# Kernel tuning notes

Hardware: AMD Instinct MI355X
Metric: run time of the kernel (lower is better)

The kernel has to match this reference:

```python
import jax, jax.numpy as jnp
import numpy as np

S = 7          # grid cells per side (CFG['CELL_NUMS'])
L_COORD = 5.0  # CFG['L_COORD']
L_NOOBJ = 0.5  # CFG['L_NOOBJ']
N_BATCH = 16384


def setup_inputs() -> dict:
    key = jax.random.key(0)
    k1, k2, k3 = jax.random.split(key, 3)
    pred = jax.random.uniform(k1, (N_BATCH, S, S, 30), dtype=jnp.float32)
    target = jax.random.uniform(k2, (N_BATCH, S, S, 30), dtype=jnp.float32)
    obj = jax.random.uniform(k3, (N_BATCH, S, S)) < 0.3
    target = target.at[..., 4].set(jnp.where(obj, target[..., 4], 0.0))
    target = target.at[..., 9].set(jnp.where(obj, target[..., 9], 0.0))
    return {"pred_tensor": pred, "target_tensor": target}


def _yolo_v1_loss(pred, target):
    # pred/target: [N, S, S, 30] = [2 boxes x (x,y,w,h,c), 20 class probs]
    N = pred.shape[0]
    coo_f = (target[..., 4] > 0).astype(pred.dtype)   # [N,S,S] object cells
    noo_f = 1.0 - coo_f                                # no-object cells

    # no-object loss: confidence channels 4 and 9 on noo cells (sum-MSE)
    nooobj_loss = jnp.sum(
        noo_f * ((pred[..., 4] - target[..., 4]) ** 2
                 + (pred[..., 9] - target[..., 9]) ** 2))

    # class loss over object cells (sum-MSE over 20 classes)
    class_loss = jnp.sum(coo_f[..., None] * (pred[..., 10:] - target[..., 10:]) ** 2)

    # boxes: [N,S,S,2,5]
    pb = pred[..., :10].reshape(N, S, S, 2, 5)
    tb = target[..., :10].reshape(N, S, S, 2, 5)

    # xywh -> xyxy for the 2 predicted boxes and the first target box per cell
    p_lt = pb[..., :2] - 0.5 * pb[..., 2:4]
    p_rb = pb[..., :2] + 0.5 * pb[..., 2:4]
    t0 = tb[..., 0, :]                                 # target box used for IOU
    t_lt = t0[..., :2] - 0.5 * t0[..., 2:4]
    t_rb = t0[..., :2] + 0.5 * t0[..., 2:4]

    # NOTE: faithful reproduction of the source's compute_iou, including its
    # bug: wh = (rb - lt < 0).float(), so 'inter' is an indicator product.
    lt = jnp.maximum(p_lt, t_lt[..., None, :])         # [N,S,S,2,2]
    rb = jnp.minimum(p_rb, t_rb[..., None, :])
    wh_ind = (rb - lt < 0).astype(pred.dtype)
    inter = wh_ind[..., 0] * wh_ind[..., 1]            # [N,S,S,2]
    area1 = (p_rb[..., 0] - p_lt[..., 0]) * (p_rb[..., 1] - p_lt[..., 1])
    area2 = ((t_rb[..., 0] - t_lt[..., 0]) * (t_rb[..., 1] - t_lt[..., 1]))[..., None]
    iou = inter / (area1 + area2 - inter)              # [N,S,S,2]

    # responsible box = argmax IOU over the 2 predicted boxes per cell
    idx = jnp.argmax(iou, axis=-1)                     # [N,S,S]
    gather = idx[..., None, None]                      # [N,S,S,1,1]
    resp_p = jnp.take_along_axis(pb, gather, axis=3)[..., 0, :]  # [N,S,S,5]
    resp_t = jnp.take_along_axis(tb, gather, axis=3)[..., 0, :]

    contain_loss = jnp.sum(coo_f * (resp_p[..., 4] - resp_t[..., 4]) ** 2)

    # guard sqrt at masked-out cells so 0*d(sqrt(0)) does not produce NaN grads
    safe = coo_f[..., None] > 0
    sqrt_wp = jnp.sqrt(jnp.where(safe, resp_p[..., 2:4], 1.0))
    sqrt_wt = jnp.sqrt(jnp.where(safe, resp_t[..., 2:4], 1.0))
    loc_loss = (jnp.sum(coo_f[..., None] * (resp_p[..., :2] - resp_t[..., :2]) ** 2)
                + jnp.sum(coo_f[..., None] * (sqrt_wp - sqrt_wt) ** 2))

    return (L_COORD * loc_loss + contain_loss + L_NOOBJ * nooobj_loss + class_loss) / N


def reference(pred_tensor, target_tensor):
    return _yolo_v1_loss(pred_tensor, target_tensor)
```

## Files before the change

### kernel.cpp

```cpp
#include <hip/hip_runtime.h>


#define CH 30
#define CPB 256
#define T 256
#define TILE_F (CPB * CH)
#define TILE_V4 (TILE_F / 4)

typedef __attribute__((address_space(3))) void* lds_vp;
typedef const __attribute__((address_space(1))) void* gvp;

__global__ __launch_bounds__(T, 4)
void yolo_partial(const float* __restrict__ pred,
                  const float* __restrict__ targ,
                  float* __restrict__ partial) {
    __shared__ float tile[TILE_F];
    __shared__ float wave_sums[T / 64];

    const int tid = threadIdx.x;
    const long long fbase = (long long)blockIdx.x * TILE_F;

    {
        const float4* gt = (const float4*)(targ + fbase);
#pragma unroll
        for (int k = 0; k < 8; ++k) {
            const int v = tid + k * T;
            if (v < TILE_V4)
                __builtin_amdgcn_global_load_lds((gvp)(gt + v), (lds_vp)(tile + v * 4),
                                                 16, 0, 0);
        }
    }
    __syncthreads();

    float2 t01, t23, t45, t67, t89, tc[10];
    {
        const float2* t2 = (const float2*)(tile + tid * CH);
        t01 = t2[0]; t23 = t2[1]; t45 = t2[2]; t67 = t2[3]; t89 = t2[4];
#pragma unroll
        for (int k = 0; k < 10; ++k) tc[k] = t2[5 + k];
    }
    __syncthreads();

    {
        const float4* gp = (const float4*)(pred + fbase);
#pragma unroll
        for (int k = 0; k < 8; ++k) {
            const int v = tid + k * T;
            if (v < TILE_V4)
                __builtin_amdgcn_global_load_lds((gvp)(gp + v), (lds_vp)(tile + v * 4),
                                                 16, 0, 0);
        }
    }
    __syncthreads();

    float sum = 0.0f;
    {
        const float2* p2 = (const float2*)(tile + tid * CH);
        const float2 p01 = p2[0], p23 = p2[1], p45 = p2[2], p67 = p2[3], p89 = p2[4];

        const float t4 = t45.x, t9 = t89.y;
        const bool coo = t4 > 0.0f;

        const float d4 = p45.x - t4;
        const float d9 = p89.y - t9;
        sum = coo ? 0.0f : 0.5f * (d4 * d4 + d9 * d9);

        if (coo) {
            float cl = 0.0f;
#pragma unroll
            for (int k = 0; k < 10; ++k) {
                const float2 pc = p2[5 + k];
                const float dx = pc.x - tc[k].x;
                const float dy = pc.y - tc[k].y;
                cl += dx * dx + dy * dy;
            }
            sum += cl;

            const float tltx = t01.x - 0.5f * t23.x;
            const float tlty = t01.y - 0.5f * t23.y;
            const float trbx = t01.x + 0.5f * t23.x;
            const float trby = t01.y + 0.5f * t23.y;
            const float area2 = (trbx - tltx) * (trby - tlty);

            const float b0x = p01.x, b0y = p01.y, b0w = p23.x, b0h = p23.y;
            const float b1x = p45.y, b1y = p67.x, b1w = p67.y, b1h = p89.x;

            float iou0, iou1;
            {
                const float pltx = b0x - 0.5f * b0w, plty = b0y - 0.5f * b0h;
                const float prbx = b0x + 0.5f * b0w, prby = b0y + 0.5f * b0h;
                const float ltx = fmaxf(pltx, tltx), lty = fmaxf(plty, tlty);
                const float rbx = fminf(prbx, trbx), rby = fminf(prby, trby);
                const float inter = ((rbx - ltx < 0.0f) ? 1.0f : 0.0f) *
                                    ((rby - lty < 0.0f) ? 1.0f : 0.0f);
                const float area1 = (prbx - pltx) * (prby - plty);
                iou0 = inter / (area1 + area2 - inter);
            }
            {
                const float pltx = b1x - 0.5f * b1w, plty = b1y - 0.5f * b1h;
                const float prbx = b1x + 0.5f * b1w, prby = b1y + 0.5f * b1h;
                const float ltx = fmaxf(pltx, tltx), lty = fmaxf(plty, tlty);
                const float rbx = fminf(prbx, trbx), rby = fminf(prby, trby);
                const float inter = ((rbx - ltx < 0.0f) ? 1.0f : 0.0f) *
                                    ((rby - lty < 0.0f) ? 1.0f : 0.0f);
                const float area1 = (prbx - pltx) * (prby - plty);
                iou1 = inter / (area1 + area2 - inter);
            }
            const bool idx1 = iou1 > iou0;

            const float rpx = idx1 ? b1x : b0x;
            const float rpy = idx1 ? b1y : b0y;
            const float rpw = idx1 ? b1w : b0w;
            const float rph = idx1 ? b1h : b0h;
            const float rpc = idx1 ? p89.y : p45.x;
            const float rtx = idx1 ? t45.y : t01.x;
            const float rty = idx1 ? t67.x : t01.y;
            const float rtw = idx1 ? t67.y : t23.x;
            const float rth = idx1 ? t89.x : t23.y;
            const float rtc = idx1 ? t89.y : t45.x;

            const float dc = rpc - rtc;
            sum += dc * dc;

            const float dx = rpx - rtx;
            const float dy = rpy - rty;
            const float dw = sqrtf(rpw) - sqrtf(rtw);
            const float dh = sqrtf(rph) - sqrtf(rth);
            sum += 5.0f * (dx * dx + dy * dy + dw * dw + dh * dh);
        }
    }

#pragma unroll
    for (int off = 32; off > 0; off >>= 1)
        sum += __shfl_down(sum, off, 64);
    const int wave = tid >> 6;
    const int lane = tid & 63;
    if (lane == 0) wave_sums[wave] = sum;
    __syncthreads();
    if (tid == 0) {
        float tot = 0.0f;
#pragma unroll
        for (int w = 0; w < T / 64; ++w) tot += wave_sums[w];
        partial[blockIdx.x] = tot;
    }
}

__global__ __launch_bounds__(256)
void yolo_reduce(const float* __restrict__ partial, int n, float* __restrict__ out) {
    __shared__ float wave_sums[4];
    float s = 0.0f;
    const int n4 = n >> 2;
    const float4* p4 = (const float4*)partial;
    for (int v = threadIdx.x; v < n4; v += 256) {
        const float4 x = p4[v];
        s += (x.x + x.y) + (x.z + x.w);
    }
    for (int v = (n4 << 2) + threadIdx.x; v < n; v += 256)
        s += partial[v];
#pragma unroll
    for (int off = 32; off > 0; off >>= 1)
        s += __shfl_down(s, off, 64);
    const int wave = threadIdx.x >> 6;
    const int lane = threadIdx.x & 63;
    if (lane == 0) wave_sums[wave] = s;
    __syncthreads();
    if (threadIdx.x == 0) {
        const float tot = wave_sums[0] + wave_sums[1] + wave_sums[2] + wave_sums[3];
        out[0] = tot * (1.0f / 16384.0f);
    }
}

extern "C" void kernel_launch(void* const* d_in, const int* in_sizes, int n_in,
                              void* d_out, int out_size, void* d_ws, size_t ws_size,
                              hipStream_t stream) {
    const float* pred = (const float*)d_in[0];
    const float* targ = (const float*)d_in[1];
    float* out = (float*)d_out;
    float* partial = (float*)d_ws;

    const int n_cells = in_sizes[0] / CH;
    const int blocks = n_cells / CPB;

    yolo_partial<<<blocks, T, 0, stream>>>(pred, targ, partial);
    yolo_reduce<<<1, 256, 0, stream>>>(partial, blocks, out);
}
```

Measured before the change: 204.5 us.

## Replace LDS-staged tile loads with direct per-thread global float2 loads

Drops the global_load_lds staging of target and pred tiles into shared memory, along with the block barriers between stages. Each thread now reads its own cell's 30 floats of target and pred directly from global memory into registers as float2 loads. This removes the LDS round trip and barriers and lets both inputs load concurrently. The cost is strided, uncoalesced per-thread access with a 120-byte stride, which spreads each wave's loads across many cache lines and relies on L2/TA efficiency.

```diff
diff --git a/kernel.cpp b/kernel.cpp
--- a/kernel.cpp
+++ b/kernel.cpp
@@ -2,132 +2,94 @@
 
 
 #define CH 30
-#define CPB 256
 #define T 256
-#define TILE_F (CPB * CH)
-#define TILE_V4 (TILE_F / 4)
-
-typedef __attribute__((address_space(3))) void* lds_vp;
-typedef const __attribute__((address_space(1))) void* gvp;
 
 __global__ __launch_bounds__(T, 4)
 void yolo_partial(const float* __restrict__ pred,
                   const float* __restrict__ targ,
                   float* __restrict__ partial) {
-    __shared__ float tile[TILE_F];
     __shared__ float wave_sums[T / 64];
 
     const int tid = threadIdx.x;
-    const long long fbase = (long long)blockIdx.x * TILE_F;
+    const size_t cell = (size_t)blockIdx.x * T + tid;
 
-    {
-        const float4* gt = (const float4*)(targ + fbase);
+    const float2* t2 = (const float2*)targ + cell * (CH / 2);
+    const float2* p2 = (const float2*)pred + cell * (CH / 2);
+
+    float2 t[15], p[15];
 #pragma unroll
-        for (int k = 0; k < 8; ++k) {
-            const int v = tid + k * T;
-            if (v < TILE_V4)
-                __builtin_amdgcn_global_load_lds((gvp)(gt + v), (lds_vp)(tile + v * 4),
-                                                 16, 0, 0);
+    for (int k = 0; k < 15; ++k) t[k] = t2[k];
+#pragma unroll
+    for (int k = 0; k < 15; ++k) p[k] = p2[k];
+
+    const float t4 = t[2].x, t9 = t[4].y;
+    const bool coo = t4 > 0.0f;
+
+    const float d4 = p[2].x - t4;
+    const float d9 = p[4].y - t9;
+    float sum = coo ? 0.0f : 0.5f * (d4 * d4 + d9 * d9);
+
+    if (coo) {
+        float cl = 0.0f;
+#pragma unroll
+        for (int k = 0; k < 10; ++k) {
+            const float dx = p[5 + k].x - t[5 + k].x;
+            const float dy = p[5 + k].y - t[5 + k].y;
+            cl += dx * dx + dy * dy;
         }
-    }
-    __syncthreads();
+        sum += cl;
 
-    float2 t01, t23, t45, t67, t89, tc[10];
-    {
-        const float2* t2 = (const float2*)(tile + tid * CH);
-        t01 = t2[0]; t23 = t2[1]; t45 = t2[2]; t67 = t2[3]; t89 = t2[4];
-#pragma unroll
-        for (int k = 0; k < 10; ++k) tc[k] = t2[5 + k];
-    }
-    __syncthreads();
+        const float tltx = t[0].x - 0.5f * t[1].x;
+        const float tlty = t[0].y - 0.5f * t[1].y;
+        const float trbx = t[0].x + 0.5f * t[1].x;
+        const float trby = t[0].y + 0.5f * t[1].y;
+        const float area2 = (trbx - tltx) * (trby - tlty);
 
-    {
-        const float4* gp = (const float4*)(pred + fbase);
-#pragma unroll
-        for (int k = 0; k < 8; ++k) {
-            const int v = tid + k * T;
-            if (v < TILE_V4)
-                __builtin_amdgcn_global_load_lds((gvp)(gp + v), (lds_vp)(tile + v * 4),
-                                                 16, 0, 0);
+        const float b0x = p[0].x, b0y = p[0].y, b0w = p[1].x, b0h = p[1].y;
+        const float b1x = p[2].y, b1y = p[3].x, b1w = p[3].y, b1h = p[4].x;
+
+        float iou0, iou1;
+        {
+            const float pltx = b0x - 0.5f * b0w, plty = b0y - 0.5f * b0h;
+            const float prbx = b0x + 0.5f * b0w, prby = b0y + 0.5f * b0h;
+            const float ltx = fmaxf(pltx, tltx), lty = fmaxf(plty, tlty);
+            const float rbx = fminf(prbx, trbx), rby = fminf(prby, trby);
+            const float inter = ((rbx - ltx < 0.0f) ? 1.0f : 0.0f) *
+                                ((rby - lty < 0.0f) ? 1.0f : 0.0f);
+            const float area1 = (prbx - pltx) * (prby - plty);
+            iou0 = inter / (area1 + area2 - inter);
         }
-    }
-    __syncthreads();
+        {
+            const float pltx = b1x - 0.5f * b1w, plty = b1y - 0.5f * b1h;
+            const float prbx = b1x + 0.5f * b1w, prby = b1y + 0.5f * b1h;
+            const float ltx = fmaxf(pltx, tltx), lty = fmaxf(plty, tlty);
+            const float rbx = fminf(prbx, trbx), rby = fminf(prby, trby);
+            const float inter = ((rbx - ltx < 0.0f) ? 1.0f : 0.0f) *
+                                ((rby - lty < 0.0f) ? 1.0f : 0.0f);
+            const float area1 = (prbx - pltx) * (prby - plty);
+            iou1 = inter / (area1 + area2 - inter);
+        }
+        const bool idx1 = iou1 > iou0;
 
-    float sum = 0.0f;
-    {
-        const float2* p2 = (const float2*)(tile + tid * CH);
-        const float2 p01 = p2[0], p23 = p2[1], p45 = p2[2], p67 = p2[3], p89 = p2[4];
+        const float rpx = idx1 ? b1x : b0x;
+        const float rpy = idx1 ? b1y : b0y;
+        const float rpw = idx1 ? b1w : b0w;
+        const float rph = idx1 ? b1h : b0h;
+        const float rpc = idx1 ? p[4].y : p[2].x;
+        const float rtx = idx1 ? t[2].y : t[0].x;
+        const float rty = idx1 ? t[3].x : t[0].y;
+        const float rtw = idx1 ? t[3].y : t[1].x;
+        const float rth = idx1 ? t[4].x : t[1].y;
+        const float rtc = idx1 ? t[4].y : t[2].x;
 
-        const float t4 = t45.x, t9 = t89.y;
-        const bool coo = t4 > 0.0f;
+        const float dc = rpc - rtc;
+        sum += dc * dc;
 
-        const float d4 = p45.x - t4;
-        const float d9 = p89.y - t9;
-        sum = coo ? 0.0f : 0.5f * (d4 * d4 + d9 * d9);
-
-        if (coo) {
-            float cl = 0.0f;
-#pragma unroll
-            for (int k = 0; k < 10; ++k) {
-                const float2 pc = p2[5 + k];
-                const float dx = pc.x - tc[k].x;
-                const float dy = pc.y - tc[k].y;
-                cl += dx * dx + dy * dy;
-            }
-            sum += cl;
-
-            const float tltx = t01.x - 0.5f * t23.x;
-            const float tlty = t01.y - 0.5f * t23.y;
-            const float trbx = t01.x + 0.5f * t23.x;
-            const float trby = t01.y + 0.5f * t23.y;
-            const float area2 = (trbx - tltx) * (trby - tlty);
-
-            const float b0x = p01.x, b0y = p01.y, b0w = p23.x, b0h = p23.y;
-            const float b1x = p45.y, b1y = p67.x, b1w = p67.y, b1h = p89.x;
-
-            float iou0, iou1;
-            {
-                const float pltx = b0x - 0.5f * b0w, plty = b0y - 0.5f * b0h;
-                const float prbx = b0x + 0.5f * b0w, prby = b0y + 0.5f * b0h;
-                const float ltx = fmaxf(pltx, tltx), lty = fmaxf(plty, tlty);
-                const float rbx = fminf(prbx, trbx), rby = fminf(prby, trby);
-                const float inter = ((rbx - ltx < 0.0f) ? 1.0f : 0.0f) *
-                                    ((rby - lty < 0.0f) ? 1.0f : 0.0f);
-                const float area1 = (prbx - pltx) * (prby - plty);
-                iou0 = inter / (area1 + area2 - inter);
-            }
-            {
-                const float pltx = b1x - 0.5f * b1w, plty = b1y - 0.5f * b1h;
-                const float prbx = b1x + 0.5f * b1w, prby = b1y + 0.5f * b1h;
-                const float ltx = fmaxf(pltx, tltx), lty = fmaxf(plty, tlty);
-                const float rbx = fminf(prbx, trbx), rby = fminf(prby, trby);
-                const float inter = ((rbx - ltx < 0.0f) ? 1.0f : 0.0f) *
-                                    ((rby - lty < 0.0f) ? 1.0f : 0.0f);
-                const float area1 = (prbx - pltx) * (prby - plty);
-                iou1 = inter / (area1 + area2 - inter);
-            }
-            const bool idx1 = iou1 > iou0;
-
-            const float rpx = idx1 ? b1x : b0x;
-            const float rpy = idx1 ? b1y : b0y;
-            const float rpw = idx1 ? b1w : b0w;
-            const float rph = idx1 ? b1h : b0h;
-            const float rpc = idx1 ? p89.y : p45.x;
-            const float rtx = idx1 ? t45.y : t01.x;
-            const float rty = idx1 ? t67.x : t01.y;
-            const float rtw = idx1 ? t67.y : t23.x;
-            const float rth = idx1 ? t89.x : t23.y;
-            const float rtc = idx1 ? t89.y : t45.x;
-
-            const float dc = rpc - rtc;
-            sum += dc * dc;
-
-            const float dx = rpx - rtx;
-            const float dy = rpy - rty;
-            const float dw = sqrtf(rpw) - sqrtf(rtw);
-            const float dh = sqrtf(rph) - sqrtf(rth);
-            sum += 5.0f * (dx * dx + dy * dy + dw * dw + dh * dh);
-        }
+        const float dx = rpx - rtx;
+        const float dy = rpy - rty;
+        const float dw = sqrtf(rpw) - sqrtf(rtw);
+        const float dh = sqrtf(rph) - sqrtf(rth);
+        sum += 5.0f * (dx * dx + dy * dy + dw * dw + dh * dh);
     }
 
 #pragma unroll
@@ -179,7 +141,7 @@
     float* partial = (float*)d_ws;
 
     const int n_cells = in_sizes[0] / CH;
-    const int blocks = n_cells / CPB;
+    const int blocks = n_cells / T;
 
     yolo_partial<<<blocks, T, 0, stream>>>(pred, targ, partial);
     yolo_reduce<<<1, 256, 0, stream>>>(partial, blocks, out);
```

Measured after the change: 206.0 us. About the same (+0.7%).
